# Kernel tuning notes

Hardware: AMD Instinct MI355X
Metric: run time of the kernel (lower is better)

Reference implementation:

```python
import jax, jax.numpy as jnp
import numpy as np

D_MODEL = 2048
NUM_HEADS = 32
NUM_KV_HEADS = 8
HEAD_DIM = D_MODEL // NUM_HEADS  # 64
KV_DIM = NUM_KV_HEADS * HEAD_DIM  # 512
B, S = 2, 2048


def setup_inputs() -> dict:
    key = jax.random.key(0)
    kx, kq, kk, kv, ko = jax.random.split(key, 5)
    sc = 0.02
    return {
        "x": jax.random.normal(kx, (B, S, D_MODEL), dtype=jnp.float32),
        "W_q": jax.random.normal(kq, (D_MODEL, D_MODEL), dtype=jnp.float32) * sc,
        "W_k": jax.random.normal(kk, (D_MODEL, KV_DIM), dtype=jnp.float32) * sc,
        "W_v": jax.random.normal(kv, (D_MODEL, KV_DIM), dtype=jnp.float32) * sc,
        "W_o": jax.random.normal(ko, (D_MODEL, D_MODEL), dtype=jnp.float32) * sc,
    }


def reference(x, W_q, W_k, W_v, W_o):
    b, s, _ = x.shape
    g = NUM_HEADS // NUM_KV_HEADS  # queries per kv head
    q = (x @ W_q).reshape(b, s, NUM_HEADS, HEAD_DIM)
    k = (x @ W_k).reshape(b, s, NUM_KV_HEADS, HEAD_DIM)
    v = (x @ W_v).reshape(b, s, NUM_KV_HEADS, HEAD_DIM)
    # repeat_interleave KV heads to match query heads
    k = jnp.repeat(k, g, axis=2)
    v = jnp.repeat(v, g, axis=2)
    # [b, h, s, d]
    q = q.transpose(0, 2, 1, 3)
    k = k.transpose(0, 2, 1, 3)
    v = v.transpose(0, 2, 1, 3)
    scores = jnp.einsum('bhqd,bhkd->bhqk', q, k) / jnp.sqrt(
        jnp.asarray(HEAD_DIM, dtype=x.dtype))
    attn = jax.nn.softmax(scores, axis=-1)
    ctx = jnp.einsum('bhqk,bhkd->bhqd', attn, v)
    ctx = ctx.transpose(0, 2, 1, 3).reshape(b, s, D_MODEL)
    return ctx @ W_o
```

## Files before the change

### kernel.cpp

```cpp
#include <hip/hip_runtime.h>

typedef float  f32x4  __attribute__((ext_vector_type(4)));
typedef float  f32x16 __attribute__((ext_vector_type(16)));
typedef short  s16x8  __attribute__((ext_vector_type(8)));
typedef unsigned short u16x8 __attribute__((ext_vector_type(8)));
typedef unsigned short u16x4 __attribute__((ext_vector_type(4)));

#define DMODEL 2048
#define NH     32
#define NKV    8
#define HD     64
#define QKVN   3072
#define SS     2048
#define BB     2

#define QSCALE 0.18033688f

__device__ __forceinline__ unsigned short f2bf(float f) {
  unsigned int u = __float_as_uint(f);
  u += 0x7fff + ((u >> 16) & 1);
  return (unsigned short)(u >> 16);
}

__device__ __forceinline__ void gload16(const void* g, void* l) {
  __builtin_amdgcn_global_load_lds((const __attribute__((address_space(1))) void*)g,
                                   (__attribute__((address_space(3))) void*)l, 16, 0, 0);
}

__device__ __forceinline__ unsigned int cvtpk(float lo, float hi) {
  unsigned int r;
  asm("v_cvt_pk_bf16_f32 %0, %1, %2" : "=v"(r) : "v"(lo), "v"(hi));
  return r;
}
__device__ __forceinline__ void plswap(unsigned int& x, unsigned int& y) {
  asm("v_permlane32_swap_b32 %0, %1" : "+v"(x), "+v"(y));
}

__global__ __launch_bounds__(256) void cast_x(const float* __restrict__ in,
                                              unsigned short* __restrict__ out) {
  int i = (blockIdx.x * 256 + threadIdx.x) * 8;
  float4 a = *(const float4*)(in + i);
  float4 b = *(const float4*)(in + i + 4);
  u16x8 r;
  r[0] = f2bf(a.x); r[1] = f2bf(a.y); r[2] = f2bf(a.z); r[3] = f2bf(a.w);
  r[4] = f2bf(b.x); r[5] = f2bf(b.y); r[6] = f2bf(b.z); r[7] = f2bf(b.w);
  *(u16x8*)(out + i) = r;
}

__global__ __launch_bounds__(256) void wcast(const float* __restrict__ in,
                                             unsigned short* __restrict__ out,
                                             int N, int K, float scale) {
  __shared__ float t[32][33];
  int n0 = blockIdx.x * 32, k0 = blockIdx.y * 32;
  int r  = threadIdx.x >> 3;
  int c4 = (threadIdx.x & 7) * 4;
  float4 v = *(const float4*)(in + (size_t)(k0 + r) * N + n0 + c4);
  t[r][c4 + 0] = v.x; t[r][c4 + 1] = v.y; t[r][c4 + 2] = v.z; t[r][c4 + 3] = v.w;
  __syncthreads();
  u16x4 o;
  o[0] = f2bf(t[c4 + 0][r] * scale);
  o[1] = f2bf(t[c4 + 1][r] * scale);
  o[2] = f2bf(t[c4 + 2][r] * scale);
  o[3] = f2bf(t[c4 + 3][r] * scale);
  *(u16x4*)(out + (size_t)(n0 + r) * K + k0 + c4) = o;
}

__global__ __launch_bounds__(256) void repack_vt(const unsigned short* __restrict__ qkv,
                                                 unsigned short* __restrict__ vt) {
  int gid = blockIdx.x * 256 + threadIdx.x;
  int d   = gid & 63;
  int sb  = (gid >> 6) & 255;
  int bk  = gid >> 14;
  int b = bk >> 3, kvh = bk & 7;
  const unsigned short* src = qkv + (size_t)(b * SS + sb * 8) * QKVN + 2560 + kvh * 64 + d;
  u16x8 r;
#pragma unroll
  for (int j = 0; j < 8; ++j) r[j] = src[(size_t)j * QKVN];
  *(u16x8*)(vt + (size_t)(bk * 64 + d) * SS + sb * 8) = r;
}

template <int BF16OUT>
__global__ __launch_bounds__(256, 2) void gemm_bt(const unsigned short* __restrict__ A,
                                                  const unsigned short* __restrict__ B,
                                                  void* __restrict__ Cv,
                                                  int M, int N, int K, int ldc) {
  __shared__ unsigned short lA[128 * 32];
  __shared__ unsigned short lB[128 * 32];
  int tid = threadIdx.x;
  int wave = tid >> 6, lane = tid & 63;

  int gx  = gridDim.x;
  int nwg = gx * gridDim.y;
  int bid = blockIdx.y * gx + blockIdx.x;
  int swz = (bid & 7) * (nwg >> 3) + (bid >> 3);
  int n0 = (swz % gx) * 128;
  int m0 = (swz / gx) * 128;

  int wr = (wave >> 1) * 64, wc = (wave & 1) * 64;
  f32x4 acc[4][4] = {};

  int rowa = wave * 32 + (lane >> 2);
  int kca  = (lane & 3) * 8;
  int loff = wave * 1024 + lane * 8;

  const unsigned short* Ag = A + (size_t)(m0 + rowa) * K + kca;
  const unsigned short* Bg = B + (size_t)(n0 + rowa) * K + kca;

  int nkt = K >> 5;
  for (int kt = 0; kt < nkt; ++kt) {
    __syncthreads();
    gload16(Ag,           lA + loff);
    gload16(Ag + 16 * K,  lA + loff + 512);
    gload16(Bg,           lB + loff);
    gload16(Bg + 16 * K,  lB + loff + 512);
    Ag += 32; Bg += 32;
    __syncthreads();
    s16x8 af[4], bfr[4];
    int kk = 8 * (lane >> 4);
#pragma unroll
    for (int i = 0; i < 4; ++i) {
      af[i]  = *(const s16x8*)&lA[(wr + i * 16 + (lane & 15)) * 32 + kk];
      bfr[i] = *(const s16x8*)&lB[(wc + i * 16 + (lane & 15)) * 32 + kk];
    }
#pragma unroll
    for (int i = 0; i < 4; ++i)
#pragma unroll
      for (int j = 0; j < 4; ++j)
        acc[i][j] = __builtin_amdgcn_mfma_f32_16x16x32_bf16(af[i], bfr[j], acc[i][j], 0, 0, 0);
  }

  int cr0 = m0 + wr + (lane >> 4) * 4;
  int cc0 = n0 + wc + (lane & 15);
  if (BF16OUT) {
    unsigned short* C = (unsigned short*)Cv;
#pragma unroll
    for (int i = 0; i < 4; ++i)
#pragma unroll
      for (int j = 0; j < 4; ++j)
#pragma unroll
        for (int r = 0; r < 4; ++r)
          C[(size_t)(cr0 + i * 16 + r) * ldc + cc0 + j * 16] = f2bf(acc[i][j][r]);
  } else {
    float* C = (float*)Cv;
#pragma unroll
    for (int i = 0; i < 4; ++i)
#pragma unroll
      for (int j = 0; j < 4; ++j)
#pragma unroll
        for (int r = 0; r < 4; ++r)
          C[(size_t)(cr0 + i * 16 + r) * ldc + cc0 + j * 16] = acc[i][j][r];
  }
}

__global__ __launch_bounds__(256, 3) void attn3(const unsigned short* __restrict__ qkv,
                                                const unsigned short* __restrict__ vt,
                                                unsigned short* __restrict__ ctxb) {
  __shared__ unsigned short sm[2][2][4096];
  int tid = threadIdx.x, wave = tid >> 6, lane = tid & 63;
  int bid = blockIdx.x;
  int swz = (bid & 7) * 128 + (bid >> 3);
  int qt = swz & 63, kvh = (swz >> 6) & 7, b = swz >> 9;
  int head = kvh * 4 + wave;
  int qs = qt * 32;
  int h = lane >> 5, q = lane & 31;

  const unsigned short* qrow = qkv + (size_t)(b * SS + qs + q) * QKVN + head * 64 + 8 * h;
  s16x8 qf[4];
#pragma unroll
  for (int ks = 0; ks < 4; ++ks) qf[ks] = *(const s16x8*)&qrow[ks * 16];

  const unsigned short* kbase = qkv + (size_t)(b * SS) * QKVN + 2048 + kvh * 64;
  const unsigned short* vbase = vt + (size_t)((b * 8 + kvh) * 64) * SS;

  int sr  = wave * 16 + (lane >> 3);
  int wch = ((lane & 7) ^ (lane >> 3)) * 8;
  int wo0 = sr * 64 + wch, wo1 = wo0 + 512;
  const unsigned short* kg0 = kbase + (size_t)sr * QKVN + (lane & 7) * 8;
  const unsigned short* vg0 = vbase + (size_t)sr * SS + (lane & 7) * 8;

  s16x8 ones;
#pragma unroll
  for (int j = 0; j < 8; ++j) ones[j] = (short)0x3F80;

  f32x16 o0 = {}, o1 = {}, o_l = {};

  {
    f32x4 k0 = *(const f32x4*)(kg0);
    f32x4 k1 = *(const f32x4*)(kg0 + 8 * QKVN);
    f32x4 v0 = *(const f32x4*)(vg0);
    f32x4 v1 = *(const f32x4*)(vg0 + 8 * SS);
    *(f32x4*)&sm[0][0][wo0] = k0;  *(f32x4*)&sm[0][0][wo1] = k1;
    *(f32x4*)&sm[0][1][wo0] = v0;  *(f32x4*)&sm[0][1][wo1] = v1;
  }
  __syncthreads();

  for (int t = 0; t < 32; ++t) {
    int cur = t & 1, nb = cur ^ 1;
    f32x4 k0, k1, v0, v1;
    if (t < 31) {
      const unsigned short* kp = kg0 + (size_t)(t + 1) * (64 * QKVN);
      const unsigned short* vp = vg0 + (t + 1) * 64;
      k0 = *(const f32x4*)(kp);
      k1 = *(const f32x4*)(kp + 8 * QKVN);
      v0 = *(const f32x4*)(vp);
      v1 = *(const f32x4*)(vp + 8 * SS);
    }
    const unsigned short* lK = sm[cur][0];
    const unsigned short* lV = sm[cur][1];

    f32x16 sa0 = {}, sa1 = {};
    __builtin_amdgcn_s_setprio(1);
#pragma unroll
    for (int ks = 0; ks < 4; ++ks) {
      s16x8 kf0 = *(const s16x8*)&lK[q * 64 + (((2 * ks + h) ^ (q & 7)) << 3)];
      sa0 = __builtin_amdgcn_mfma_f32_32x32x16_bf16(kf0, qf[ks], sa0, 0, 0, 0);
    }
#pragma unroll
    for (int ks = 0; ks < 4; ++ks) {
      s16x8 kf1 = *(const s16x8*)&lK[(q + 32) * 64 + (((2 * ks + h) ^ (q & 7)) << 3)];
      sa1 = __builtin_amdgcn_mfma_f32_32x32x16_bf16(kf1, qf[ks], sa1, 0, 0, 0);
    }
    __builtin_amdgcn_s_setprio(0);

#pragma unroll
    for (int r = 0; r < 16; ++r) sa0[r] = exp2f(sa0[r]);
#pragma unroll
    for (int r = 0; r < 16; ++r) sa1[r] = exp2f(sa1[r]);

    union PW { s16x8 v; unsigned int w[4]; };
    PW pa[4];
#pragma unroll
    for (int kb = 0; kb < 2; ++kb)
#pragma unroll
      for (int sub = 0; sub < 2; ++sub) {
        const f32x16& s = kb ? sa1 : sa0;
        int base = sub * 8;
        unsigned int x0 = cvtpk(s[base + 0], s[base + 1]);
        unsigned int y0 = cvtpk(s[base + 4], s[base + 5]);
        plswap(x0, y0);
        unsigned int x1 = cvtpk(s[base + 2], s[base + 3]);
        unsigned int y1 = cvtpk(s[base + 6], s[base + 7]);
        plswap(x1, y1);
        PW& p = pa[kb * 2 + sub];
        p.w[0] = x0; p.w[1] = x1; p.w[2] = y0; p.w[3] = y1;
      }

    __builtin_amdgcn_s_setprio(1);
#pragma unroll
    for (int ks = 0; ks < 4; ++ks)
      o_l = __builtin_amdgcn_mfma_f32_32x32x16_bf16(ones, pa[ks].v, o_l, 0, 0, 0);
#pragma unroll
    for (int ks = 0; ks < 4; ++ks) {
      s16x8 vf0 = *(const s16x8*)&lV[q * 64 + (((2 * ks + h) ^ (q & 7)) << 3)];
      o0 = __builtin_amdgcn_mfma_f32_32x32x16_bf16(vf0, pa[ks].v, o0, 0, 0, 0);
      s16x8 vf1 = *(const s16x8*)&lV[(q + 32) * 64 + (((2 * ks + h) ^ (q & 7)) << 3)];
      o1 = __builtin_amdgcn_mfma_f32_32x32x16_bf16(vf1, pa[ks].v, o1, 0, 0, 0);
    }
    __builtin_amdgcn_s_setprio(0);

    if (t < 31) {
      *(f32x4*)&sm[nb][0][wo0] = k0;  *(f32x4*)&sm[nb][0][wo1] = k1;
      *(f32x4*)&sm[nb][1][wo0] = v0;  *(f32x4*)&sm[nb][1][wo1] = v1;
    }
    __syncthreads();
  }

  float invl = 1.0f / o_l[0];
  unsigned short* lT = (unsigned short*)&sm[0][0][0] + wave * 2048;
#pragma unroll
  for (int db = 0; db < 2; ++db)
#pragma unroll
    for (int r = 0; r < 16; r += 2) {
      int d = (r & 3) + 8 * (r >> 2) + 4 * h + 32 * db;
      float lo = (db ? o1[r] : o0[r]) * invl;
      float hi = (db ? o1[r + 1] : o0[r + 1]) * invl;
      *(unsigned int*)&lT[q * 64 + (((d >> 3) ^ (q & 7)) << 3) + (d & 7)] = cvtpk(lo, hi);
    }
  __syncthreads();
  unsigned short* cb = ctxb + (size_t)(b * SS + qs) * DMODEL + head * 64;
#pragma unroll
  for (int c = 0; c < 4; ++c) {
    int cc = h * 4 + c;
    u16x8 v = *(const u16x8*)&lT[q * 64 + ((cc ^ (q & 7)) << 3)];
    *(u16x8*)&cb[(size_t)q * DMODEL + cc * 8] = v;
  }
}

extern "C" void kernel_launch(void* const* d_in, const int* in_sizes, int n_in,
                              void* d_out, int out_size, void* d_ws, size_t ws_size,
                              hipStream_t stream) {
  (void)in_sizes; (void)n_in; (void)out_size; (void)ws_size;
  const float* x  = (const float*)d_in[0];
  const float* Wq = (const float*)d_in[1];
  const float* Wk = (const float*)d_in[2];
  const float* Wv = (const float*)d_in[3];
  const float* Wo = (const float*)d_in[4];
  float* out = (float*)d_out;

  char* ws = (char*)d_ws;
  unsigned short* xb    = (unsigned short*)(ws);
  unsigned short* ctxb  = xb;
  unsigned short* wqkvT = (unsigned short*)(ws + 16777216);
  unsigned short* vtb   = wqkvT;
  unsigned short* woT   = (unsigned short*)(ws + 29360128);
  unsigned short* qkv   = (unsigned short*)(ws + 37748736);

  cast_x<<<4096, 256, 0, stream>>>(x, xb);
  {
    dim3 g(64, 64); wcast<<<g, 256, 0, stream>>>(Wq, wqkvT, 2048, 2048, QSCALE);
  }
  {
    dim3 g(16, 64);
    wcast<<<g, 256, 0, stream>>>(Wk, wqkvT + (size_t)2048 * 2048, 512, 2048, 1.0f);
    wcast<<<g, 256, 0, stream>>>(Wv, wqkvT + (size_t)2560 * 2048, 512, 2048, 1.0f);
  }
  {
    dim3 g(64, 64); wcast<<<g, 256, 0, stream>>>(Wo, woT, 2048, 2048, 1.0f);
  }
  {
    dim3 g(24, 32);
    gemm_bt<1><<<g, 256, 0, stream>>>(xb, wqkvT, qkv, 4096, 3072, 2048, 3072);
  }
  repack_vt<<<1024, 256, 0, stream>>>(qkv, vtb);
  attn3<<<1024, 256, 0, stream>>>(qkv, vtb, ctxb);
  {
    dim3 g(16, 32);
    gemm_bt<0><<<g, 256, 0, stream>>>(ctxb, woT, out, 4096, 2048, 2048, 2048);
  }
}
```

Measured before the change: 339.0 us.

## Split attention waves by head pair and key half; tile V transpose via LDS

The attention kernel now assigns each wave two query heads and half of each 64-key tile, rather than one head and the full tile. Each K fragment read from LDS is reused across two heads. The ones-matrix MFMA that computed the row sum is replaced with scalar adds plus a cross-half shuffle, and partial outputs and sums are reduced through a 64KB LDS scratch at the end. The V transpose kernel now stages 64x64 tiles in shared memory so that reads and writes are coalesced. In exchange, occupancy drops to 2 blocks per CU, LDS use rises, and there is an extra reduction epilogue.

```diff
diff --git a/kernel.cpp b/kernel.cpp
--- a/kernel.cpp
+++ b/kernel.cpp
@@ -65,18 +65,29 @@
   *(u16x4*)(out + (size_t)(n0 + r) * K + k0 + c4) = o;
 }
 
-__global__ __launch_bounds__(256) void repack_vt(const unsigned short* __restrict__ qkv,
-                                                 unsigned short* __restrict__ vt) {
-  int gid = blockIdx.x * 256 + threadIdx.x;
-  int d   = gid & 63;
-  int sb  = (gid >> 6) & 255;
-  int bk  = gid >> 14;
+__global__ __launch_bounds__(256) void repack_vt2(const unsigned short* __restrict__ qkv,
+                                                  unsigned short* __restrict__ vt) {
+  __shared__ unsigned short lt[64][66];
+  int bk = blockIdx.y, s0 = blockIdx.x * 64;
   int b = bk >> 3, kvh = bk & 7;
-  const unsigned short* src = qkv + (size_t)(b * SS + sb * 8) * QKVN + 2560 + kvh * 64 + d;
-  u16x8 r;
-#pragma unroll
-  for (int j = 0; j < 8; ++j) r[j] = src[(size_t)j * QKVN];
-  *(u16x8*)(vt + (size_t)(bk * 64 + d) * SS + sb * 8) = r;
+  int tid = threadIdx.x;
+  int r = tid >> 2, c = tid & 3;
+  const unsigned short* src = qkv + (size_t)(b * SS + s0 + r) * QKVN + 2560 + kvh * 64;
+#pragma unroll
+  for (int i = 0; i < 2; ++i) {
+    int ch = c + i * 4;
+    u16x8 v = *(const u16x8*)(src + ch * 8);
+#pragma unroll
+    for (int j = 0; j < 8; ++j) lt[ch * 8 + j][r] = v[j];
+  }
+  __syncthreads();
+  int d = tid >> 2;
+  unsigned short* dst = vt + (size_t)(bk * 64 + d) * SS + s0;
+#pragma unroll
+  for (int i = 0; i < 2; ++i) {
+    int ch = c + i * 4;
+    *(u16x8*)(dst + ch * 8) = *(const u16x8*)&lt[d][ch * 8];
+  }
 }
 
 template <int BF16OUT>
@@ -152,22 +163,27 @@
   }
 }
 
-__global__ __launch_bounds__(256, 3) void attn3(const unsigned short* __restrict__ qkv,
+__global__ __launch_bounds__(256, 2) void attn4(const unsigned short* __restrict__ qkv,
                                                 const unsigned short* __restrict__ vt,
                                                 unsigned short* __restrict__ ctxb) {
-  __shared__ unsigned short sm[2][2][4096];
+  __shared__ __align__(16) unsigned char smraw[65536];
+  __shared__ float lred[4][2][32];
+  unsigned short* stg = (unsigned short*)smraw;
   int tid = threadIdx.x, wave = tid >> 6, lane = tid & 63;
+  int hp = wave >> 1, kh = wave & 1;
   int bid = blockIdx.x;
   int swz = (bid & 7) * 128 + (bid >> 3);
   int qt = swz & 63, kvh = (swz >> 6) & 7, b = swz >> 9;
-  int head = kvh * 4 + wave;
   int qs = qt * 32;
   int h = lane >> 5, q = lane & 31;
 
-  const unsigned short* qrow = qkv + (size_t)(b * SS + qs + q) * QKVN + head * 64 + 8 * h;
-  s16x8 qf[4];
-#pragma unroll
-  for (int ks = 0; ks < 4; ++ks) qf[ks] = *(const s16x8*)&qrow[ks * 16];
+  const unsigned short* qrow = qkv + (size_t)(b * SS + qs + q) * QKVN + (kvh * 4 + hp * 2) * 64 + 8 * h;
+  s16x8 qf[2][4];
+#pragma unroll
+  for (int j = 0; j < 2; ++j)
+#pragma unroll
+    for (int ks = 0; ks < 4; ++ks)
+      qf[j][ks] = *(const s16x8*)&qrow[j * 64 + ks * 16];
 
   const unsigned short* kbase = qkv + (size_t)(b * SS) * QKVN + 2048 + kvh * 64;
   const unsigned short* vbase = vt + (size_t)((b * 8 + kvh) * 64) * SS;
@@ -178,110 +194,155 @@
   const unsigned short* kg0 = kbase + (size_t)sr * QKVN + (lane & 7) * 8;
   const unsigned short* vg0 = vbase + (size_t)sr * SS + (lane & 7) * 8;
 
-  s16x8 ones;
-#pragma unroll
-  for (int j = 0; j < 8; ++j) ones[j] = (short)0x3F80;
-
-  f32x16 o0 = {}, o1 = {}, o_l = {};
+  f32x16 o00 = {}, o01 = {}, o10 = {}, o11 = {};
+  float l0 = 0.f, l1 = 0.f;
 
   {
     f32x4 k0 = *(const f32x4*)(kg0);
     f32x4 k1 = *(const f32x4*)(kg0 + 8 * QKVN);
     f32x4 v0 = *(const f32x4*)(vg0);
     f32x4 v1 = *(const f32x4*)(vg0 + 8 * SS);
-    *(f32x4*)&sm[0][0][wo0] = k0;  *(f32x4*)&sm[0][0][wo1] = k1;
-    *(f32x4*)&sm[0][1][wo0] = v0;  *(f32x4*)&sm[0][1][wo1] = v1;
-  }
-  __syncthreads();
+    *(f32x4*)&stg[wo0] = k0;          *(f32x4*)&stg[wo1] = k1;
+    *(f32x4*)&stg[4096 + wo0] = v0;   *(f32x4*)&stg[4096 + wo1] = v1;
+  }
+  __syncthreads();
+
+  int kq = kh * 32 + q;
+  union PW { s16x8 v; unsigned int w[4]; };
 
   for (int t = 0; t < 32; ++t) {
-    int cur = t & 1, nb = cur ^ 1;
+    unsigned short* bufc = stg + (t & 1) * 8192;
+    unsigned short* bufn = stg + ((t & 1) ^ 1) * 8192;
     f32x4 k0, k1, v0, v1;
     if (t < 31) {
       const unsigned short* kp = kg0 + (size_t)(t + 1) * (64 * QKVN);
-      const unsigned short* vp = vg0 + (t + 1) * 64;
+      const unsigned short* vp = vg0 + (size_t)(t + 1) * 64;
       k0 = *(const f32x4*)(kp);
       k1 = *(const f32x4*)(kp + 8 * QKVN);
       v0 = *(const f32x4*)(vp);
       v1 = *(const f32x4*)(vp + 8 * SS);
     }
-    const unsigned short* lK = sm[cur][0];
-    const unsigned short* lV = sm[cur][1];
-
+
+    s16x8 kf[4];
+#pragma unroll
+    for (int ks = 0; ks < 4; ++ks)
+      kf[ks] = *(const s16x8*)&bufc[kq * 64 + (((2 * ks + h) ^ (q & 7)) << 3)];
     f32x16 sa0 = {}, sa1 = {};
     __builtin_amdgcn_s_setprio(1);
 #pragma unroll
-    for (int ks = 0; ks < 4; ++ks) {
-      s16x8 kf0 = *(const s16x8*)&lK[q * 64 + (((2 * ks + h) ^ (q & 7)) << 3)];
-      sa0 = __builtin_amdgcn_mfma_f32_32x32x16_bf16(kf0, qf[ks], sa0, 0, 0, 0);
-    }
-#pragma unroll
-    for (int ks = 0; ks < 4; ++ks) {
-      s16x8 kf1 = *(const s16x8*)&lK[(q + 32) * 64 + (((2 * ks + h) ^ (q & 7)) << 3)];
-      sa1 = __builtin_amdgcn_mfma_f32_32x32x16_bf16(kf1, qf[ks], sa1, 0, 0, 0);
-    }
+    for (int ks = 0; ks < 4; ++ks)
+      sa0 = __builtin_amdgcn_mfma_f32_32x32x16_bf16(kf[ks], qf[0][ks], sa0, 0, 0, 0);
+#pragma unroll
+    for (int ks = 0; ks < 4; ++ks)
+      sa1 = __builtin_amdgcn_mfma_f32_32x32x16_bf16(kf[ks], qf[1][ks], sa1, 0, 0, 0);
     __builtin_amdgcn_s_setprio(0);
 
 #pragma unroll
-    for (int r = 0; r < 16; ++r) sa0[r] = exp2f(sa0[r]);
-#pragma unroll
-    for (int r = 0; r < 16; ++r) sa1[r] = exp2f(sa1[r]);
-
-    union PW { s16x8 v; unsigned int w[4]; };
-    PW pa[4];
-#pragma unroll
-    for (int kb = 0; kb < 2; ++kb)
-#pragma unroll
-      for (int sub = 0; sub < 2; ++sub) {
-        const f32x16& s = kb ? sa1 : sa0;
-        int base = sub * 8;
-        unsigned int x0 = cvtpk(s[base + 0], s[base + 1]);
-        unsigned int y0 = cvtpk(s[base + 4], s[base + 5]);
+    for (int r = 0; r < 16; ++r) sa0[r] = __builtin_amdgcn_exp2f(sa0[r]);
+#pragma unroll
+    for (int r = 0; r < 16; ++r) sa1[r] = __builtin_amdgcn_exp2f(sa1[r]);
+    l0 += (((sa0[0] + sa0[1]) + (sa0[2] + sa0[3])) + ((sa0[4] + sa0[5]) + (sa0[6] + sa0[7])))
+        + (((sa0[8] + sa0[9]) + (sa0[10] + sa0[11])) + ((sa0[12] + sa0[13]) + (sa0[14] + sa0[15])));
+    l1 += (((sa1[0] + sa1[1]) + (sa1[2] + sa1[3])) + ((sa1[4] + sa1[5]) + (sa1[6] + sa1[7])))
+        + (((sa1[8] + sa1[9]) + (sa1[10] + sa1[11])) + ((sa1[12] + sa1[13]) + (sa1[14] + sa1[15])));
+
+    PW pa0[2], pa1[2];
+#pragma unroll
+    for (int sub = 0; sub < 2; ++sub) {
+      int base = sub * 8;
+      {
+        unsigned int x0 = cvtpk(sa0[base + 0], sa0[base + 1]);
+        unsigned int y0 = cvtpk(sa0[base + 4], sa0[base + 5]);
         plswap(x0, y0);
-        unsigned int x1 = cvtpk(s[base + 2], s[base + 3]);
-        unsigned int y1 = cvtpk(s[base + 6], s[base + 7]);
+        unsigned int x1 = cvtpk(sa0[base + 2], sa0[base + 3]);
+        unsigned int y1 = cvtpk(sa0[base + 6], sa0[base + 7]);
         plswap(x1, y1);
-        PW& p = pa[kb * 2 + sub];
-        p.w[0] = x0; p.w[1] = x1; p.w[2] = y0; p.w[3] = y1;
+        pa0[sub].w[0] = x0; pa0[sub].w[1] = x1; pa0[sub].w[2] = y0; pa0[sub].w[3] = y1;
       }
-
+      {
+        unsigned int x0 = cvtpk(sa1[base + 0], sa1[base + 1]);
+        unsigned int y0 = cvtpk(sa1[base + 4], sa1[base + 5]);
+        plswap(x0, y0);
+        unsigned int x1 = cvtpk(sa1[base + 2], sa1[base + 3]);
+        unsigned int y1 = cvtpk(sa1[base + 6], sa1[base + 7]);
+        plswap(x1, y1);
+        pa1[sub].w[0] = x0; pa1[sub].w[1] = x1; pa1[sub].w[2] = y0; pa1[sub].w[3] = y1;
+      }
+    }
+
+    s16x8 vf[2][2];
+#pragma unroll
+    for (int ks2 = 0; ks2 < 2; ++ks2)
+#pragma unroll
+      for (int dh = 0; dh < 2; ++dh)
+        vf[ks2][dh] = *(const s16x8*)&bufc[4096 + (dh * 32 + q) * 64 +
+                                           (((kh * 4 + ks2 * 2 + h) ^ (q & 7)) << 3)];
     __builtin_amdgcn_s_setprio(1);
-#pragma unroll
-    for (int ks = 0; ks < 4; ++ks)
-      o_l = __builtin_amdgcn_mfma_f32_32x32x16_bf16(ones, pa[ks].v, o_l, 0, 0, 0);
-#pragma unroll
-    for (int ks = 0; ks < 4; ++ks) {
-      s16x8 vf0 = *(const s16x8*)&lV[q * 64 + (((2 * ks + h) ^ (q & 7)) << 3)];
-      o0 = __builtin_amdgcn_mfma_f32_32x32x16_bf16(vf0, pa[ks].v, o0, 0, 0, 0);
-      s16x8 vf1 = *(const s16x8*)&lV[(q + 32) * 64 + (((2 * ks + h) ^ (q & 7)) << 3)];
-      o1 = __builtin_amdgcn_mfma_f32_32x32x16_bf16(vf1, pa[ks].v, o1, 0, 0, 0);
-    }
+    o00 = __builtin_amdgcn_mfma_f32_32x32x16_bf16(vf[0][0], pa0[0].v, o00, 0, 0, 0);
+    o00 = __builtin_amdgcn_mfma_f32_32x32x16_bf16(vf[1][0], pa0[1].v, o00, 0, 0, 0);
+    o01 = __builtin_amdgcn_mfma_f32_32x32x16_bf16(vf[0][1], pa0[0].v, o01, 0, 0, 0);
+    o01 = __builtin_amdgcn_mfma_f32_32x32x16_bf16(vf[1][1], pa0[1].v, o01, 0, 0, 0);
+    o10 = __builtin_amdgcn_mfma_f32_32x32x16_bf16(vf[0][0], pa1[0].v, o10, 0, 0, 0);
+    o10 = __builtin_amdgcn_mfma_f32_32x32x16_bf16(vf[1][0], pa1[1].v, o10, 0, 0, 0);
+    o11 = __builtin_amdgcn_mfma_f32_32x32x16_bf16(vf[0][1], pa1[0].v, o11, 0, 0, 0);
+    o11 = __builtin_amdgcn_mfma_f32_32x32x16_bf16(vf[1][1], pa1[1].v, o11, 0, 0, 0);
     __builtin_amdgcn_s_setprio(0);
 
     if (t < 31) {
-      *(f32x4*)&sm[nb][0][wo0] = k0;  *(f32x4*)&sm[nb][0][wo1] = k1;
-      *(f32x4*)&sm[nb][1][wo0] = v0;  *(f32x4*)&sm[nb][1][wo1] = v1;
+      *(f32x4*)&bufn[wo0] = k0;          *(f32x4*)&bufn[wo1] = k1;
+      *(f32x4*)&bufn[4096 + wo0] = v0;   *(f32x4*)&bufn[4096 + wo1] = v1;
     }
     __syncthreads();
   }
 
-  float invl = 1.0f / o_l[0];
-  unsigned short* lT = (unsigned short*)&sm[0][0][0] + wave * 2048;
+  l0 += __shfl_xor(l0, 32);
+  l1 += __shfl_xor(l1, 32);
+  float* scr = (float*)smraw;
+
+#pragma unroll
+  for (int j = 0; j < 2; ++j)
+#pragma unroll
+    for (int db = 0; db < 2; ++db)
+#pragma unroll
+      for (int r = 0; r < 16; ++r) {
+        int d = (r & 3) + 8 * (r >> 2) + 4 * h + 32 * db;
+        float v = (j == 0) ? (db ? o01[r] : o00[r]) : (db ? o11[r] : o10[r]);
+        scr[(wave * 2 + j) * 2048 + d * 32 + q] = v;
+      }
+  if (h == 0) { lred[wave][0][q] = l0; lred[wave][1][q] = l1; }
+  __syncthreads();
+
+  int jj  = wave & 1;
+  int sbA = (hp * 2 + 0) * 2 + jj;
+  int sbB = (hp * 2 + 1) * 2 + jj;
+  float of[2][16];
+#pragma unroll
+  for (int db = 0; db < 2; ++db)
+#pragma unroll
+    for (int r = 0; r < 16; ++r) {
+      int d = (r & 3) + 8 * (r >> 2) + 4 * h + 32 * db;
+      of[db][r] = scr[sbA * 2048 + d * 32 + q] + scr[sbB * 2048 + d * 32 + q];
+    }
+  float lt = lred[hp * 2][jj][q] + lred[hp * 2 + 1][jj][q];
+  float invl = 1.0f / lt;
+  __syncthreads();
+
+  unsigned short* tb = (unsigned short*)smraw + wave * 2048;
 #pragma unroll
   for (int db = 0; db < 2; ++db)
 #pragma unroll
     for (int r = 0; r < 16; r += 2) {
       int d = (r & 3) + 8 * (r >> 2) + 4 * h + 32 * db;
-      float lo = (db ? o1[r] : o0[r]) * invl;
-      float hi = (db ? o1[r + 1] : o0[r + 1]) * invl;
-      *(unsigned int*)&lT[q * 64 + (((d >> 3) ^ (q & 7)) << 3) + (d & 7)] = cvtpk(lo, hi);
-    }
-  __syncthreads();
-  unsigned short* cb = ctxb + (size_t)(b * SS + qs) * DMODEL + head * 64;
+      *(unsigned int*)&tb[q * 64 + (((d >> 3) ^ (q & 7)) << 3) + (d & 7)] =
+          cvtpk(of[db][r] * invl, of[db][r + 1] * invl);
+    }
+  __syncthreads();
+
+  unsigned short* cb = ctxb + (size_t)(b * SS + qs) * DMODEL + (kvh * 4 + wave) * 64;
 #pragma unroll
   for (int c = 0; c < 4; ++c) {
     int cc = h * 4 + c;
-    u16x8 v = *(const u16x8*)&lT[q * 64 + ((cc ^ (q & 7)) << 3)];
+    u16x8 v = *(const u16x8*)&tb[q * 64 + ((cc ^ (q & 7)) << 3)];
     *(u16x8*)&cb[(size_t)q * DMODEL + cc * 8] = v;
   }
 }
@@ -321,8 +382,11 @@
     dim3 g(24, 32);
     gemm_bt<1><<<g, 256, 0, stream>>>(xb, wqkvT, qkv, 4096, 3072, 2048, 3072);
   }
-  repack_vt<<<1024, 256, 0, stream>>>(qkv, vtb);
-  attn3<<<1024, 256, 0, stream>>>(qkv, vtb, ctxb);
+  {
+    dim3 g(32, 16);
+    repack_vt2<<<g, 256, 0, stream>>>(qkv, vtb);
+  }
+  attn4<<<1024, 256, 0, stream>>>(qkv, vtb, ctxb);
   {
     dim3 g(16, 32);
     gemm_bt<0><<<g, 256, 0, stream>>>(ctxb, woT, out, 4096, 2048, 2048, 2048);
```

Measured after the change: 309.6 us. 8.7% less time.
